# Kernel optimization log

Hardware: AMD Instinct MI355X
Metric: run time of the kernel (lower is better)

The kernel has to match this reference:

```python
import jax, jax.numpy as jnp
import numpy as np

V = 50257
D = 512
T = 1024


def setup_inputs() -> dict:
    key = jax.random.key(0)
    ks = jax.random.split(key, 12)
    si = (2.0 / (V + D)) ** 0.5   # xavier-ish scale for input matrices
    sh = (1.0 / D) ** 0.5         # scale for recurrent matrices
    so = (2.0 / (V + D)) ** 0.5
    return {
        "idx": jax.random.randint(ks[0], (T,), 0, V, dtype=jnp.int32),
        "W_ii": jax.random.normal(ks[1], (D, V), jnp.float32) * si,
        "W_if": jax.random.normal(ks[2], (D, V), jnp.float32) * si,
        "W_io": jax.random.normal(ks[3], (D, V), jnp.float32) * si,
        "W_ig": jax.random.normal(ks[4], (D, V), jnp.float32) * si,
        "W_hi": jax.random.normal(ks[5], (D, D), jnp.float32) * sh,
        "W_hf": jax.random.normal(ks[6], (D, D), jnp.float32) * sh,
        "W_ho": jax.random.normal(ks[7], (D, D), jnp.float32) * sh,
        "W_hg": jax.random.normal(ks[8], (D, D), jnp.float32) * sh,
        "b_i": jnp.zeros((D,), jnp.float32),
        "b_f": jnp.ones((D,), jnp.float32),
        "b_o": jnp.zeros((D,), jnp.float32),
        "b_g": jnp.zeros((D,), jnp.float32),
        "W_out": jax.random.normal(ks[9], (V, D), jnp.float32) * so,
        "b_out": jnp.zeros((V,), jnp.float32),
    }


def reference(idx, W_ii, W_if, W_io, W_ig, W_hi, W_hf, W_ho, W_hg,
              b_i, b_f, b_o, b_g, W_out, b_out):
    # One-hot @ W.T == column gather: W[:, tok]. Dropout is identity (eval mode).
    dims = W_hi.shape[0]

    def step(carry, tok):
        h, c = carry
        i = jax.nn.sigmoid(W_ii[:, tok] + b_i + W_hi @ h)
        f = jax.nn.sigmoid(W_if[:, tok] + b_f + W_hf @ h)
        o = jax.nn.sigmoid(W_io[:, tok] + b_o + W_ho @ h)
        g = jnp.tanh(W_ig[:, tok] + b_g + W_hg @ h)
        c_new = f * c + i * g
        h_new = o * jnp.tanh(c_new)
        logits = W_out @ h_new + b_out          # [V]
        return (h_new, c_new), jax.nn.log_softmax(logits)

    h0 = jnp.zeros((dims,), W_hi.dtype)
    c0 = jnp.zeros((dims,), W_hi.dtype)
    (h, c), log_probs = jax.lax.scan(step, (h0, c0), idx)
    return log_probs, h, c  # log_probs: [T, V]
```

## Files before the change

kernel.cpp:

```cpp
#include <hip/hip_runtime.h>
#include <hip/hip_bf16.h>

#define VV 50257
#define DD 512
#define TT 1024
#define VPADN 50304
#define NBR 64
#define WCB 128

typedef __bf16 bf16;
typedef __attribute__((ext_vector_type(8))) __bf16 bf16x8;
typedef __attribute__((ext_vector_type(4))) __bf16 bf16x4;
typedef __attribute__((ext_vector_type(4))) float f32x4;

__device__ __forceinline__ void gload_lds16(const void* g, void* l) {
  __builtin_amdgcn_global_load_lds(
      (__attribute__((address_space(1))) void*)(void*)g,
      (__attribute__((address_space(3))) void*)l, 16, 0, 0);
}

__global__ __launch_bounds__(512) __attribute__((amdgpu_waves_per_eu(2, 2)))
void recur_fused_kernel(
    const int* __restrict__ idx,
    const float* __restrict__ Wii, const float* __restrict__ Wif,
    const float* __restrict__ Wio, const float* __restrict__ Wig,
    const float* __restrict__ Whi, const float* __restrict__ Whf,
    const float* __restrict__ Who, const float* __restrict__ Whg,
    const float* __restrict__ bi, const float* __restrict__ bfv,
    const float* __restrict__ bo, const float* __restrict__ bg,
    const float* __restrict__ Wout,
    unsigned long long* __restrict__ Hpack, bf16* __restrict__ Hbf,
    bf16* __restrict__ Wbf, float* __restrict__ out_tail) {
  __shared__ float hsh[2][DD];
  __shared__ int idxs[TT];
  const int b = blockIdx.x, tid = threadIdx.x;

  if (b >= NBR) {
    const int wb = b - NBR;
    const size_t nch = (size_t)VPADN * DD / 4;
    for (size_t i = (size_t)wb * 512 + tid; i < nch; i += (size_t)WCB * 512) {
      size_t e = i << 2;
      bf16x4 o;
      if ((e >> 9) < VV) {
        f32x4 x = *(const f32x4*)&Wout[e];
        o[0] = (bf16)x[0]; o[1] = (bf16)x[1]; o[2] = (bf16)x[2]; o[3] = (bf16)x[3];
      } else {
        o[0] = o[1] = o[2] = o[3] = (bf16)0.f;
      }
      *(bf16x4*)&Wbf[e] = o;
    }
    return;
  }

  idxs[tid] = idx[tid];
  idxs[tid + 512] = idx[tid + 512];

  const int lane = tid & 63, w = tid >> 6;
  const int hd = (b << 3) + w;

  f32x4 wr0[4], wr1[4];
  {
    #pragma unroll
    for (int g = 0; g < 4; ++g) {
      const float* Wg = (g == 0) ? Whi : (g == 1) ? Whf : (g == 2) ? Who : Whg;
      wr0[g] = *(const f32x4*)&Wg[(size_t)hd*DD + (lane << 2)];
      wr1[g] = *(const f32x4*)&Wg[(size_t)hd*DD + 256 + (lane << 2)];
    }
  }
  #pragma unroll
  for (int g = 0; g < 4; ++g) {
    asm volatile("" : "+v"(wr0[g]));
    asm volatile("" : "+v"(wr1[g]));
  }

  const float* wxp = nullptr;
  float bias = 0.f;
  if (lane < 4) {
    const float* Wx = (lane == 0) ? Wii : (lane == 1) ? Wif : (lane == 2) ? Wio : Wig;
    const float* bx = (lane == 0) ? bi : (lane == 1) ? bfv : (lane == 2) ? bo : bg;
    wxp = &Wx[(size_t)hd * VV];
    bias = bx[hd];
  }
  float c = 0.f;
  __syncthreads();

  for (int t = 0; t < TT; ++t) {
    float xv = 0.f;
    if (lane < 4) xv = wxp[idxs[t]] + bias;

    float* hb = hsh[t & 1];
    if (t > 0) {
      const unsigned long long* src = &Hpack[(size_t)(t-1)*DD + tid];
      unsigned long long v;
      do {
        asm volatile("global_load_dwordx2 %0, %1, off sc1\n\t"
                     "s_waitcnt vmcnt(0)"
                     : "=v"(v) : "v"(src) : "memory");
      } while (__builtin_expect((unsigned)(v >> 32) != (unsigned)t, 0));
      hb[tid] = __uint_as_float((unsigned)v);
    } else {
      hb[tid] = 0.f;
    }
    __syncthreads();

    const f32x4 h0 = *(const f32x4*)&hb[lane << 2];
    const f32x4 h1 = *(const f32x4*)&hb[256 + (lane << 2)];
    f32x4 m0 = wr0[0]*h0 + wr1[0]*h1;
    f32x4 m1 = wr0[1]*h0 + wr1[1]*h1;
    f32x4 m2 = wr0[2]*h0 + wr1[2]*h1;
    f32x4 m3 = wr0[3]*h0 + wr1[3]*h1;
    float a0 = m0[0]+m0[1]+m0[2]+m0[3];
    float a1 = m1[0]+m1[1]+m1[2]+m1[3];
    float a2 = m2[0]+m2[1]+m2[2]+m2[3];
    float a3 = m3[0]+m3[1]+m3[2]+m3[3];
    #pragma unroll
    for (int mask = 1; mask < 64; mask <<= 1) {
      a0 += __shfl_xor(a0, mask);
      a1 += __shfl_xor(a1, mask);
      a2 += __shfl_xor(a2, mask);
      a3 += __shfl_xor(a3, mask);
    }

    float myacc = (lane == 0) ? a0 : (lane == 1) ? a1 : (lane == 2) ? a2 : a3;
    float pre = myacc + xv;
    bool isg = (lane == 3);
    float e1 = __expf(isg ? -2.f * pre : -pre);
    float rr = 1.f / (1.f + e1);
    float act = isg ? (2.f * rr - 1.f) : rr;

    float ia = __shfl(act, 0);
    float fa = __shfl(act, 1);
    float oa = __shfl(act, 2);
    float ga = __shfl(act, 3);

    if (lane == 0) {
      c = fa * c + ia * ga;
      float e2 = __expf(-2.f * c);
      float th = 2.f / (1.f + e2) - 1.f;
      float h = oa * th;
      unsigned long long pk =
          ((unsigned long long)(unsigned)(t + 1) << 32) | (unsigned long long)__float_as_uint(h);
      __hip_atomic_store(&Hpack[(size_t)t*DD + hd], pk, __ATOMIC_RELAXED,
                         __HIP_MEMORY_SCOPE_AGENT);
      Hbf[(size_t)t*DD + hd] = (bf16)h;
      if (t == TT - 1) { out_tail[hd] = h; out_tail[DD + hd] = c; }
    }
  }
}

__global__ __launch_bounds__(256, 2) void gemm_kernel(
    const bf16* __restrict__ A, const bf16* __restrict__ B,
    const float* __restrict__ bout, float* __restrict__ Cout) {
  __shared__ bf16 As[128*32];
  __shared__ bf16 Bs[128*32];
  const int tid = threadIdx.x;
  const int n0 = blockIdx.x * 128, m0 = blockIdx.y * 128;
  const int w = tid >> 6, l = tid & 63;
  const int wr = w >> 1, wc = w & 1;
  f32x4 acc[4][4] = {};

  for (int k0 = 0; k0 < DD; k0 += 32) {
    #pragma unroll
    for (int c = 0; c < 2; ++c) {
      int j = c*256 + tid;
      int row = j >> 2, kc = (j & 3) << 3;
      gload_lds16(&A[(size_t)(m0 + row)*DD + k0 + kc], (char*)As + (c*4096 + w*1024));
      gload_lds16(&B[(size_t)(n0 + row)*DD + k0 + kc], (char*)Bs + (c*4096 + w*1024));
    }
    __syncthreads();
    bf16x8 af[4], bfr[4];
    #pragma unroll
    for (int mi = 0; mi < 4; ++mi)
      af[mi] = *(const bf16x8*)&As[(wr*64 + mi*16 + (l & 15))*32 + (l >> 4)*8];
    #pragma unroll
    for (int ni = 0; ni < 4; ++ni)
      bfr[ni] = *(const bf16x8*)&Bs[(wc*64 + ni*16 + (l & 15))*32 + (l >> 4)*8];
    #pragma unroll
    for (int mi = 0; mi < 4; ++mi)
      #pragma unroll
      for (int ni = 0; ni < 4; ++ni)
        acc[mi][ni] = __builtin_amdgcn_mfma_f32_16x16x32_bf16(af[mi], bfr[ni], acc[mi][ni], 0, 0, 0);
    __syncthreads();
  }

  #pragma unroll
  for (int mi = 0; mi < 4; ++mi) {
    int rbase = m0 + wr*64 + mi*16 + (l >> 4)*4;
    #pragma unroll
    for (int ni = 0; ni < 4; ++ni) {
      int col = n0 + wc*64 + ni*16 + (l & 15);
      if (col < VV) {
        float bb = bout[col];
        #pragma unroll
        for (int r = 0; r < 4; ++r)
          Cout[(size_t)(rbase + r)*VV + col] = acc[mi][ni][r] + bb;
      }
    }
  }
}

__global__ __launch_bounds__(256) void lsm_kernel(float* __restrict__ logits) {
  const int t = blockIdx.x, tid = threadIdx.x;
  float* row = logits + (size_t)t*VV;
  float m = -INFINITY, s = 0.f;
  for (int v = tid; v < VV; v += 256) {
    float x = row[v];
    float nm = fmaxf(m, x);
    s = s*expf(m - nm) + expf(x - nm);
    m = nm;
  }
  #pragma unroll
  for (int mask = 1; mask < 64; mask <<= 1) {
    float om = __shfl_xor(m, mask);
    float os = __shfl_xor(s, mask);
    float nm = fmaxf(m, om);
    s = s*expf(m - nm) + os*expf(om - nm);
    m = nm;
  }
  __shared__ float sm[4], ss[4], lse_sh;
  int wv = tid >> 6;
  if ((tid & 63) == 0) { sm[wv] = m; ss[wv] = s; }
  __syncthreads();
  if (tid == 0) {
    float M = sm[0], S = ss[0];
    for (int i2 = 1; i2 < 4; ++i2) {
      float nm = fmaxf(M, sm[i2]);
      S = S*expf(M - nm) + ss[i2]*expf(sm[i2] - nm);
      M = nm;
    }
    lse_sh = M + logf(S);
  }
  __syncthreads();
  float lse = lse_sh;
  for (int v = tid; v < VV; v += 256)
    row[v] -= lse;
}

extern "C" void kernel_launch(void* const* d_in, const int* in_sizes, int n_in,
                              void* d_out, int out_size, void* d_ws, size_t ws_size,
                              hipStream_t stream) {
  const int*   idx  = (const int*)d_in[0];
  const float* Wii  = (const float*)d_in[1];
  const float* Wif  = (const float*)d_in[2];
  const float* Wio  = (const float*)d_in[3];
  const float* Wig  = (const float*)d_in[4];
  const float* Whi  = (const float*)d_in[5];
  const float* Whf  = (const float*)d_in[6];
  const float* Who  = (const float*)d_in[7];
  const float* Whg  = (const float*)d_in[8];
  const float* bi   = (const float*)d_in[9];
  const float* bfv  = (const float*)d_in[10];
  const float* bo   = (const float*)d_in[11];
  const float* bg   = (const float*)d_in[12];
  const float* Wout = (const float*)d_in[13];
  const float* bout = (const float*)d_in[14];
  float* out = (float*)d_out;

  char* ws = (char*)d_ws;
  bf16*  Wbf  = (bf16*)ws;
  unsigned long long* Hpack = (unsigned long long*)(ws + 51511296);
  bf16*  Hbf  = (bf16*)(ws + 55705600);

  hipMemsetAsync(Hpack, 0, (size_t)TT*DD*8, stream);
  recur_fused_kernel<<<NBR + WCB, 512, 0, stream>>>(
      idx, Wii, Wif, Wio, Wig, Whi, Whf, Who, Whg, bi, bfv, bo, bg, Wout,
      Hpack, Hbf, Wbf, out + (size_t)TT*VV);
  gemm_kernel<<<dim3(393, 8), 256, 0, stream>>>(Hbf, Wbf, bout, out);
  lsm_kernel<<<TT, 256, 0, stream>>>(out);
}
```

Baseline: 2.061 ms.

## Poll hidden state directly into registers per wave, drop LDS barrier

Each wave now loads the full previous hidden vector straight from the global packed buffer into registers with vectorized polling loads, instead of one element per thread staged through LDS followed by a block-wide __syncthreads. The loads for the next step and the next input-weight gather are issued early, right after the current step's store, so their latency overlaps. The gate reduction is rewritten as a transpose-style butterfly that needs fewer shuffles. The cost is that every wave issues redundant global reads of all 512 values per step, and correctness relies on the manual vmcnt waits in inline asm.

```diff
diff --git a/kernel.cpp b/kernel.cpp
--- a/kernel.cpp
+++ b/kernel.cpp
@@ -12,12 +12,15 @@
 typedef __attribute__((ext_vector_type(8))) __bf16 bf16x8;
 typedef __attribute__((ext_vector_type(4))) __bf16 bf16x4;
 typedef __attribute__((ext_vector_type(4))) float f32x4;
+typedef __attribute__((ext_vector_type(4))) unsigned int u32x4;
 
 __device__ __forceinline__ void gload_lds16(const void* g, void* l) {
   __builtin_amdgcn_global_load_lds(
       (__attribute__((address_space(1))) void*)(void*)g,
       (__attribute__((address_space(3))) void*)l, 16, 0, 0);
 }
+
+__device__ __forceinline__ unsigned umin2(unsigned a, unsigned b) { return a < b ? a : b; }
 
 __global__ __launch_bounds__(512) __attribute__((amdgpu_waves_per_eu(2, 2)))
 void recur_fused_kernel(
@@ -31,7 +34,6 @@
     const float* __restrict__ Wout,
     unsigned long long* __restrict__ Hpack, bf16* __restrict__ Hbf,
     bf16* __restrict__ Wbf, float* __restrict__ out_tail) {
-  __shared__ float hsh[2][DD];
   __shared__ int idxs[TT];
   const int b = blockIdx.x, tid = threadIdx.x;
 
@@ -81,30 +83,42 @@
     wxp = &Wx[(size_t)hd * VV];
     bias = bx[hd];
   }
-  float c = 0.f;
+  float c = 0.f, hout = 0.f;
   __syncthreads();
 
+  const float bias_my = __shfl(bias, lane & 3);
+  float xv_cur = 0.f;
+  if (lane < 4) xv_cur = wxp[idxs[0]];
+
+  u32x4 p0, p1, p2, p3;
+  const unsigned long long* lo = nullptr;
+  const unsigned long long* hi = nullptr;
+  f32x4 h0 = {0.f, 0.f, 0.f, 0.f}, h1 = {0.f, 0.f, 0.f, 0.f};
+
   for (int t = 0; t < TT; ++t) {
-    float xv = 0.f;
-    if (lane < 4) xv = wxp[idxs[t]] + bias;
-
-    float* hb = hsh[t & 1];
     if (t > 0) {
-      const unsigned long long* src = &Hpack[(size_t)(t-1)*DD + tid];
-      unsigned long long v;
-      do {
-        asm volatile("global_load_dwordx2 %0, %1, off sc1\n\t"
+      asm volatile("s_waitcnt vmcnt(0)" ::: "memory");
+      __builtin_amdgcn_sched_barrier(0);
+      unsigned mn = umin2(umin2(umin2(p0[1], p0[3]), umin2(p1[1], p1[3])),
+                          umin2(umin2(p2[1], p2[3]), umin2(p3[1], p3[3])));
+      while (__builtin_expect(mn != (unsigned)t, 0)) {
+        asm volatile("global_load_dwordx4 %0, %4, off sc1\n\t"
+                     "global_load_dwordx4 %1, %4, off offset:16 sc1\n\t"
+                     "global_load_dwordx4 %2, %5, off sc1\n\t"
+                     "global_load_dwordx4 %3, %5, off offset:16 sc1\n\t"
                      "s_waitcnt vmcnt(0)"
-                     : "=v"(v) : "v"(src) : "memory");
-      } while (__builtin_expect((unsigned)(v >> 32) != (unsigned)t, 0));
-      hb[tid] = __uint_as_float((unsigned)v);
-    } else {
-      hb[tid] = 0.f;
-    }
-    __syncthreads();
-
-    const f32x4 h0 = *(const f32x4*)&hb[lane << 2];
-    const f32x4 h1 = *(const f32x4*)&hb[256 + (lane << 2)];
+                     : "=&v"(p0), "=&v"(p1), "=&v"(p2), "=&v"(p3)
+                     : "v"(lo), "v"(hi) : "memory");
+        __builtin_amdgcn_sched_barrier(0);
+        mn = umin2(umin2(umin2(p0[1], p0[3]), umin2(p1[1], p1[3])),
+                   umin2(umin2(p2[1], p2[3]), umin2(p3[1], p3[3])));
+      }
+      h0[0] = __uint_as_float(p0[0]); h0[1] = __uint_as_float(p0[2]);
+      h0[2] = __uint_as_float(p1[0]); h0[3] = __uint_as_float(p1[2]);
+      h1[0] = __uint_as_float(p2[0]); h1[1] = __uint_as_float(p2[2]);
+      h1[2] = __uint_as_float(p3[0]); h1[3] = __uint_as_float(p3[2]);
+    }
+
     f32x4 m0 = wr0[0]*h0 + wr1[0]*h1;
     f32x4 m1 = wr0[1]*h0 + wr1[1]*h1;
     f32x4 m2 = wr0[2]*h0 + wr1[2]*h1;
@@ -113,39 +127,62 @@
     float a1 = m1[0]+m1[1]+m1[2]+m1[3];
     float a2 = m2[0]+m2[1]+m2[2]+m2[3];
     float a3 = m3[0]+m3[1]+m3[2]+m3[3];
-    #pragma unroll
-    for (int mask = 1; mask < 64; mask <<= 1) {
-      a0 += __shfl_xor(a0, mask);
-      a1 += __shfl_xor(a1, mask);
-      a2 += __shfl_xor(a2, mask);
-      a3 += __shfl_xor(a3, mask);
-    }
-
-    float myacc = (lane == 0) ? a0 : (lane == 1) ? a1 : (lane == 2) ? a2 : a3;
-    float pre = myacc + xv;
-    bool isg = (lane == 3);
+
+    float s01 = (lane & 1) ? a1 : a0;
+    float o01 = (lane & 1) ? a0 : a1;
+    s01 += __shfl_xor(o01, 1);
+    float s23 = (lane & 1) ? a3 : a2;
+    float o23 = (lane & 1) ? a2 : a3;
+    s23 += __shfl_xor(o23, 1);
+    float ss = (lane & 2) ? s23 : s01;
+    float oo = (lane & 2) ? s01 : s23;
+    ss += __shfl_xor(oo, 2);
+    ss += __shfl_xor(ss, 4);
+    ss += __shfl_xor(ss, 8);
+    ss += __shfl_xor(ss, 16);
+    ss += __shfl_xor(ss, 32);
+
+    float pre = ss + __shfl(xv_cur, lane & 3) + bias_my;
+    bool isg = (lane & 3) == 3;
     float e1 = __expf(isg ? -2.f * pre : -pre);
     float rr = 1.f / (1.f + e1);
     float act = isg ? (2.f * rr - 1.f) : rr;
 
-    float ia = __shfl(act, 0);
     float fa = __shfl(act, 1);
     float oa = __shfl(act, 2);
     float ga = __shfl(act, 3);
 
     if (lane == 0) {
-      c = fa * c + ia * ga;
+      c = fa * c + act * ga;
       float e2 = __expf(-2.f * c);
       float th = 2.f / (1.f + e2) - 1.f;
-      float h = oa * th;
+      hout = oa * th;
       unsigned long long pk =
-          ((unsigned long long)(unsigned)(t + 1) << 32) | (unsigned long long)__float_as_uint(h);
+          ((unsigned long long)(unsigned)(t + 1) << 32) | (unsigned long long)__float_as_uint(hout);
       __hip_atomic_store(&Hpack[(size_t)t*DD + hd], pk, __ATOMIC_RELAXED,
                          __HIP_MEMORY_SCOPE_AGENT);
-      Hbf[(size_t)t*DD + hd] = (bf16)h;
-      if (t == TT - 1) { out_tail[hd] = h; out_tail[DD + hd] = c; }
-    }
-  }
+      Hbf[(size_t)t*DD + hd] = (bf16)hout;
+    }
+
+    if (t + 1 < TT) {
+      lo = &Hpack[(size_t)t*DD + ((size_t)lane << 2)];
+      hi = lo + 256;
+      asm volatile("global_load_dwordx4 %0, %4, off sc1\n\t"
+                   "global_load_dwordx4 %1, %4, off offset:16 sc1\n\t"
+                   "global_load_dwordx4 %2, %5, off sc1\n\t"
+                   "global_load_dwordx4 %3, %5, off offset:16 sc1"
+                   : "=&v"(p0), "=&v"(p1), "=&v"(p2), "=&v"(p3)
+                   : "v"(lo), "v"(hi) : "memory");
+      float xv_nxt = 0.f;
+      if (lane < 4) {
+        const float* xp = &wxp[idxs[t + 1]];
+        asm volatile("global_load_dword %0, %1, off" : "=v"(xv_nxt) : "v"(xp) : "memory");
+      }
+      xv_cur = xv_nxt;
+    }
+  }
+
+  if (lane == 0) { out_tail[hd] = hout; out_tail[DD + hd] = c; }
 }
 
 __global__ __launch_bounds__(256, 2) void gemm_kernel(
```

New measurement: 6.322 ms. +206.7%, slower.

## Stage GEMM epilogue through LDS for vector stores; vectorize log-softmax

Applied to the files above, without the earlier changes.

The GEMM epilogue now writes each wave's 16x64 accumulator tile to LDS and reads it back row-contiguous, so the logits can be written with 16-byte global stores instead of scattered scalar stores. The log-softmax kernel moves to 512 threads, handles the unaligned head and tail of each row separately and processes the aligned middle as float4, using fast __expf. This targets the memory-bound logits write and the two passes over the 200 MB logits tensor. The cost is extra LDS traffic and an LDS buffer in the GEMM, and slightly less precise exponentials.

```diff
diff --git a/kernel.cpp b/kernel.cpp
--- a/kernel.cpp
+++ b/kernel.cpp
@@ -61,16 +61,16 @@
   f32x4 wr0[4], wr1[4];
   {
     #pragma unroll
-    for (int g = 0; g < 4; ++g) {
-      const float* Wg = (g == 0) ? Whi : (g == 1) ? Whf : (g == 2) ? Who : Whg;
-      wr0[g] = *(const f32x4*)&Wg[(size_t)hd*DD + (lane << 2)];
-      wr1[g] = *(const f32x4*)&Wg[(size_t)hd*DD + 256 + (lane << 2)];
+    for (int gg = 0; gg < 4; ++gg) {
+      const float* Wg = (gg == 0) ? Whi : (gg == 1) ? Whf : (gg == 2) ? Who : Whg;
+      wr0[gg] = *(const f32x4*)&Wg[(size_t)hd*DD + (lane << 2)];
+      wr1[gg] = *(const f32x4*)&Wg[(size_t)hd*DD + 256 + (lane << 2)];
     }
   }
   #pragma unroll
-  for (int g = 0; g < 4; ++g) {
-    asm volatile("" : "+v"(wr0[g]));
-    asm volatile("" : "+v"(wr1[g]));
+  for (int gg = 0; gg < 4; ++gg) {
+    asm volatile("" : "+v"(wr0[gg]));
+    asm volatile("" : "+v"(wr1[gg]));
   }
 
   const float* wxp = nullptr;
@@ -81,7 +81,7 @@
     wxp = &Wx[(size_t)hd * VV];
     bias = bx[hd];
   }
-  float c = 0.f;
+  float c = 0.f, hout = 0.f;
   __syncthreads();
 
   for (int t = 0; t < TT; ++t) {
@@ -137,13 +137,14 @@
       c = fa * c + ia * ga;
       float e2 = __expf(-2.f * c);
       float th = 2.f / (1.f + e2) - 1.f;
-      float h = oa * th;
+      hout = oa * th;
       unsigned long long pk =
-          ((unsigned long long)(unsigned)(t + 1) << 32) | (unsigned long long)__float_as_uint(h);
+          ((unsigned long long)(unsigned)(t + 1) << 32) |
+          (unsigned long long)__float_as_uint(hout);
       __hip_atomic_store(&Hpack[(size_t)t*DD + hd], pk, __ATOMIC_RELAXED,
                          __HIP_MEMORY_SCOPE_AGENT);
-      Hbf[(size_t)t*DD + hd] = (bf16)h;
-      if (t == TT - 1) { out_tail[hd] = h; out_tail[DD + hd] = c; }
+      Hbf[(size_t)t*DD + hd] = (bf16)hout;
+      if (t == TT - 1) { out_tail[hd] = hout; out_tail[DD + hd] = c; }
     }
   }
 }
@@ -153,6 +154,7 @@
     const float* __restrict__ bout, float* __restrict__ Cout) {
   __shared__ bf16 As[128*32];
   __shared__ bf16 Bs[128*32];
+  __shared__ float Cs[4][16][72];
   const int tid = threadIdx.x;
   const int n0 = blockIdx.x * 128, m0 = blockIdx.y * 128;
   const int w = tid >> 6, l = tid & 63;
@@ -183,30 +185,62 @@
     __syncthreads();
   }
 
+  float bbv[4];
+  #pragma unroll
+  for (int ni = 0; ni < 4; ++ni) {
+    int col = n0 + wc*64 + ni*16 + (l & 15);
+    bbv[ni] = (col < VV) ? bout[col] : 0.f;
+  }
+
   #pragma unroll
   for (int mi = 0; mi < 4; ++mi) {
-    int rbase = m0 + wr*64 + mi*16 + (l >> 4)*4;
-    #pragma unroll
-    for (int ni = 0; ni < 4; ++ni) {
-      int col = n0 + wc*64 + ni*16 + (l & 15);
-      if (col < VV) {
-        float bb = bout[col];
+    #pragma unroll
+    for (int ni = 0; ni < 4; ++ni)
+      #pragma unroll
+      for (int r = 0; r < 4; ++r)
+        Cs[w][(l >> 4)*4 + r][ni*16 + (l & 15)] = acc[mi][ni][r] + bbv[ni];
+    const int rbase = m0 + wr*64 + mi*16;
+    #pragma unroll
+    for (int i = 0; i < 4; ++i) {
+      int idx2 = i*64 + l;
+      int row = idx2 >> 4, quad = idx2 & 15;
+      int col = n0 + wc*64 + quad*4;
+      f32x4 v = *(const f32x4*)&Cs[w][row][quad*4];
+      float* dst = &Cout[(size_t)(rbase + row)*VV + col];
+      if (col + 3 < VV) {
+        asm volatile("global_store_dwordx4 %0, %1, off"
+                     :: "v"(dst), "v"(v) : "memory");
+      } else {
         #pragma unroll
-        for (int r = 0; r < 4; ++r)
-          Cout[(size_t)(rbase + r)*VV + col] = acc[mi][ni][r] + bb;
+        for (int e = 0; e < 4; ++e)
+          if (col + e < VV) dst[e] = v[e];
       }
     }
   }
 }
 
-__global__ __launch_bounds__(256) void lsm_kernel(float* __restrict__ logits) {
+__global__ __launch_bounds__(512) void lsm_kernel(float* __restrict__ logits) {
   const int t = blockIdx.x, tid = threadIdx.x;
   float* row = logits + (size_t)t*VV;
+  const size_t base = (size_t)t * VV;
+  const int head = (int)((4 - (base & 3)) & 3);
+  const int nvec = (VV - head) >> 2;
+  const int tail0 = head + (nvec << 2);
+
   float m = -INFINITY, s = 0.f;
-  for (int v = tid; v < VV; v += 256) {
-    float x = row[v];
-    float nm = fmaxf(m, x);
-    s = s*expf(m - nm) + expf(x - nm);
+  if (tid < head) {
+    float x = row[tid];
+    m = x; s = 1.f;
+  } else if (tid >= 508 && (tail0 + (tid - 508)) < VV) {
+    float x = row[tail0 + (tid - 508)];
+    m = x; s = 1.f;
+  }
+  for (int i = tid; i < nvec; i += 512) {
+    f32x4 x = *(const f32x4*)&row[head + (i << 2)];
+    float mx = fmaxf(fmaxf(x[0], x[1]), fmaxf(x[2], x[3]));
+    float nm = fmaxf(m, mx);
+    s = s*__expf(m - nm) + __expf(x[0] - nm) + __expf(x[1] - nm)
+        + __expf(x[2] - nm) + __expf(x[3] - nm);
     m = nm;
   }
   #pragma unroll
@@ -214,26 +248,32 @@
     float om = __shfl_xor(m, mask);
     float os = __shfl_xor(s, mask);
     float nm = fmaxf(m, om);
-    s = s*expf(m - nm) + os*expf(om - nm);
+    s = s*__expf(m - nm) + os*__expf(om - nm);
     m = nm;
   }
-  __shared__ float sm[4], ss[4], lse_sh;
+  __shared__ float sm[8], ss[8], lse_sh;
   int wv = tid >> 6;
   if ((tid & 63) == 0) { sm[wv] = m; ss[wv] = s; }
   __syncthreads();
   if (tid == 0) {
     float M = sm[0], S = ss[0];
-    for (int i2 = 1; i2 < 4; ++i2) {
+    for (int i2 = 1; i2 < 8; ++i2) {
       float nm = fmaxf(M, sm[i2]);
-      S = S*expf(M - nm) + ss[i2]*expf(sm[i2] - nm);
+      S = S*__expf(M - nm) + ss[i2]*__expf(sm[i2] - nm);
       M = nm;
     }
     lse_sh = M + logf(S);
   }
   __syncthreads();
   float lse = lse_sh;
-  for (int v = tid; v < VV; v += 256)
-    row[v] -= lse;
+  if (tid < head) row[tid] -= lse;
+  else if (tid >= 508 && (tail0 + (tid - 508)) < VV) row[tail0 + (tid - 508)] -= lse;
+  for (int i = tid; i < nvec; i += 512) {
+    float* p = &row[head + (i << 2)];
+    f32x4 x = *(const f32x4*)p;
+    x[0] -= lse; x[1] -= lse; x[2] -= lse; x[3] -= lse;
+    *(f32x4*)p = x;
+  }
 }
 
 extern "C" void kernel_launch(void* const* d_in, const int* in_sizes, int n_in,
@@ -266,5 +306,5 @@
       idx, Wii, Wif, Wio, Wig, Whi, Whf, Who, Whg, bi, bfv, bo, bg, Wout,
       Hpack, Hbf, Wbf, out + (size_t)TT*VV);
   gemm_kernel<<<dim3(393, 8), 256, 0, stream>>>(Hbf, Wbf, bout, out);
-  lsm_kernel<<<TT, 256, 0, stream>>>(out);
-}
+  lsm_kernel<<<TT, 512, 0, stream>>>(out);
+}
```

Result: faster. 1.980 ms (-3.9%).
